# Performance work log

Hardware: AMD Instinct MI355X
Metric: run time of the kernel (lower is better)

## Reference

```python
import jax, jax.numpy as jnp
import numpy as np

B, T, V = 4096, 32, 256          # batch, decode steps, vocab
E, CE, H, L, NH = 768, 64, 256, 2, 4  # eword_dim, char_emb_dim, hidden, gru layers, heads
HD = H // NH                      # head dim
BOS, PAD = 1, 0


def _gru_cell(x, h, w_ih, w_hh, b_ih, b_hh):
    # PyTorch GRUCell math: gates ordered (r, z, n)
    gi = x @ w_ih.T + b_ih
    gh = h @ w_hh.T + b_hh
    ir, iz, inn = jnp.split(gi, 3, axis=-1)
    hr, hz, hn = jnp.split(gh, 3, axis=-1)
    r = jax.nn.sigmoid(ir + hr)
    z = jax.nn.sigmoid(iz + hz)
    n = jnp.tanh(inn + r * hn)
    return (1.0 - z) * n + z * h


def setup_inputs() -> dict:
    key = jax.random.key(0)
    ks = jax.random.split(key, 24)
    s = 0.02
    p = lambda k, shp: (jax.random.normal(k, shp, jnp.float32) * s)
    return {
        "eword": jax.random.normal(ks[0], (B, E), jnp.float32),
        "target_ids": jax.random.randint(ks[1], (B, T), 0, V),
        # params
        "char_emb": p(ks[2], (V, CE)).at[PAD].set(0.0),
        "eword_proj_w": p(ks[3], (H, E)), "eword_proj_b": p(ks[4], (H,)),
        "gru_w_ih0": p(ks[5], (3 * H, CE + E)), "gru_w_hh0": p(ks[6], (3 * H, H)),
        "gru_b_ih0": p(ks[7], (3 * H,)), "gru_b_hh0": p(ks[8], (3 * H,)),
        "gru_w_ih1": p(ks[9], (3 * H, H)), "gru_w_hh1": p(ks[10], (3 * H, H)),
        "gru_b_ih1": p(ks[11], (3 * H,)), "gru_b_hh1": p(ks[12], (3 * H,)),
        "attn_in_w": p(ks[13], (3 * H, H)), "attn_in_b": p(ks[14], (3 * H,)),
        "attn_out_w": p(ks[15], (H, H)), "attn_out_b": p(ks[16], (H,)),
        "key_w": p(ks[17], (H, E)), "key_b": p(ks[18], (H,)),
        "val_w": p(ks[19], (H, E)), "val_b": p(ks[20], (H,)),
        "proj_w": p(ks[21], (V, H)), "proj_b": p(ks[22], (V,)),
    }


def reference(eword, target_ids, char_emb, eword_proj_w, eword_proj_b,
              gru_w_ih0, gru_w_hh0, gru_b_ih0, gru_b_hh0,
              gru_w_ih1, gru_w_hh1, gru_b_ih1, gru_b_hh1,
              attn_in_w, attn_in_b, attn_out_w, attn_out_b,
              key_w, key_b, val_w, val_b, proj_w, proj_b):
    batch = eword.shape[0]
    # init hidden: tanh(Linear(eword)) broadcast across layers
    h0 = jnp.tanh(eword @ eword_proj_w.T + eword_proj_b)
    # pre-projected key/value (seq len 1), then MHA in-proj for k,v (static)
    wq, wk, wv = jnp.split(attn_in_w, 3, axis=0)
    bq, bk, bv = jnp.split(attn_in_b, 3)
    ek = (eword @ key_w.T + key_b) @ wk.T + bk        # (B, H)
    ev = (eword @ val_w.T + val_b) @ wv.T + bv        # (B, H)
    kh = ek.reshape(batch, NH, HD)                     # (B, NH, HD)
    vh = ev.reshape(batch, NH, HD)
    scale = 1.0 / np.sqrt(HD).astype(np.float32)

    # teacher forcing: input at step t is BOS for t=0, else target_ids[:, t-1]
    in_ids = jnp.concatenate(
        [jnp.full((batch, 1), BOS, target_ids.dtype), target_ids[:, :-1]], axis=1)

    def step(carry, ids):
        h_l0, h_l1 = carry
        ce = char_emb[ids] * (ids != PAD)[:, None].astype(char_emb.dtype)
        x = jnp.concatenate([ce, eword], axis=-1)     # (B, CE+E)
        h_l0 = _gru_cell(x, h_l0, gru_w_ih0, gru_w_hh0, gru_b_ih0, gru_b_hh0)
        h_l1 = _gru_cell(h_l0, h_l1, gru_w_ih1, gru_w_hh1, gru_b_ih1, gru_b_hh1)
        # single-query cross-attention over a length-1 key/value
        q = (h_l1 @ wq.T + bq).reshape(batch, NH, HD)
        score = jnp.sum(q * kh, axis=-1, keepdims=True) * scale  # (B, NH, 1)
        w = jax.nn.softmax(score, axis=-1)            # ones (len-1 softmax)
        attn = (w * vh).reshape(batch, H)
        attn_out = attn @ attn_out_w.T + attn_out_b
        out = h_l1 + attn_out
        logits = out @ proj_w.T + proj_b              # (B, V)
        return (h_l0, h_l1), logits

    _, logits_t = jax.lax.scan(step, (h0, h0), in_ids.T)  # (T, B, V)
    return jnp.transpose(logits_t, (1, 0, 2))              # (B, T, V)
```

## Files before the change

kernel.cpp:

```cpp
#include <hip/hip_runtime.h>


typedef __bf16 bf16;
typedef __attribute__((ext_vector_type(8))) __bf16 bf16x8;
typedef __attribute__((ext_vector_type(4))) __bf16 bf16x4;
typedef __attribute__((ext_vector_type(4))) float fx4;

#define MFMA16(a, b, c) __builtin_amdgcn_mfma_f32_16x16x32_bf16(a, b, c, 0, 0, 0)

__device__ __forceinline__ float sigm(float x) { return 1.0f / (1.0f + expf(-x)); }

__device__ __forceinline__ bf16x8 cvt8(const float* __restrict__ p) {
    float4 u = ((const float4*)p)[0];
    float4 v = ((const float4*)p)[1];
    bf16x8 r;
    r[0] = (bf16)u.x; r[1] = (bf16)u.y; r[2] = (bf16)u.z; r[3] = (bf16)u.w;
    r[4] = (bf16)v.x; r[5] = (bf16)v.y; r[6] = (bf16)v.z; r[7] = (bf16)v.w;
    return r;
}

__device__ __forceinline__ bf16x8 addcvt8(bf16x8 h, const float* __restrict__ p) {
    float4 u = ((const float4*)p)[0];
    float4 v = ((const float4*)p)[1];
    bf16x8 r;
    r[0] = (bf16)((float)h[0] + u.x); r[1] = (bf16)((float)h[1] + u.y);
    r[2] = (bf16)((float)h[2] + u.z); r[3] = (bf16)((float)h[3] + u.w);
    r[4] = (bf16)((float)h[4] + v.x); r[5] = (bf16)((float)h[5] + v.y);
    r[6] = (bf16)((float)h[6] + v.z); r[7] = (bf16)((float)h[7] + v.w);
    return r;
}

__global__ void f2b(const float* __restrict__ s, bf16* __restrict__ d, int n) {
    int i = (blockIdx.x * 256 + threadIdx.x) * 4;
    if (i >= n) return;
    float4 v = *(const float4*)(s + i);
    bf16x4 o;
    o[0] = (bf16)v.x; o[1] = (bf16)v.y; o[2] = (bf16)v.z; o[3] = (bf16)v.w;
    *(bf16x4*)(d + i) = o;
}

__global__ __launch_bounds__(256, 4) void gemm_bt(
    const float* __restrict__ A, int lda,
    const float* __restrict__ W, int ldw,
    const float* __restrict__ bias,
    float* __restrict__ out, int ldo, int act_tanh, int K)
{
    const int tid  = threadIdx.x;
    const int wid  = tid >> 6;
    const int lane = tid & 63;
    const int quad = lane >> 4;
    const int l16  = lane & 15;
    const int m0   = blockIdx.x * 32;
    const int n0   = blockIdx.y * 256 + wid * 64;

    fx4 acc[4][2];
#pragma unroll
    for (int j = 0; j < 4; ++j) {
        acc[j][0] = fx4{0.f, 0.f, 0.f, 0.f};
        acc[j][1] = fx4{0.f, 0.f, 0.f, 0.f};
    }

    const float* a0p = A + (size_t)(m0 + l16) * lda + quad * 8;
    const float* a1p = A + (size_t)(m0 + 16 + l16) * lda + quad * 8;

    for (int k0 = 0; k0 < K; k0 += 32) {
        bf16x8 a0 = cvt8(a0p + k0);
        bf16x8 a1 = cvt8(a1p + k0);
#pragma unroll
        for (int j = 0; j < 4; ++j) {
            bf16x8 b = cvt8(W + (size_t)(n0 + j * 16 + l16) * ldw + k0 + quad * 8);
            acc[j][0] = MFMA16(a0, b, acc[j][0]);
            acc[j][1] = MFMA16(a1, b, acc[j][1]);
        }
    }

#pragma unroll
    for (int j = 0; j < 4; ++j) {
        int n = n0 + j * 16 + l16;
        float bv = bias ? bias[n] : 0.0f;
#pragma unroll
        for (int rt = 0; rt < 2; ++rt)
#pragma unroll
            for (int r = 0; r < 4; ++r) {
                int m = m0 + rt * 16 + quad * 4 + r;
                float v = acc[j][rt][r] + bv;
                if (act_tanh) v = tanhf(v);
                out[(size_t)m * ldo + n] = v;
            }
    }
}

__global__ __launch_bounds__(1024) void decoder_loop(
    const int*   __restrict__ tgt,
    const float* __restrict__ h0i,
    const float* __restrict__ gword,
    const float* __restrict__ cproj,
    const bf16*  __restrict__ w_hh0, const float* __restrict__ b_hh0,
    const bf16*  __restrict__ w_ih1, const float* __restrict__ b_ih1,
    const bf16*  __restrict__ w_hh1, const float* __restrict__ b_hh1,
    bf16* __restrict__ h1all)
{
    __shared__ __align__(16) bf16 hb0[2][16][264];
    __shared__ __align__(16) bf16 hb1[2][16][264];

    const int tid  = threadIdx.x;
    const int wid  = tid >> 6;
    const int lane = tid & 63;
    const int quad = lane >> 4;
    const int l16  = lane & 15;
    const int row0 = blockIdx.x * 16;
    const int col  = wid * 16 + l16;

    float h0m[4], h1m[4], gwv[3][4], cpv[3][4];
    float bh0[3], bi1[3], bh1[3];
#pragma unroll
    for (int g = 0; g < 3; ++g) {
        bh0[g] = b_hh0[g * 256 + col];
        bi1[g] = b_ih1[g * 256 + col];
        bh1[g] = b_hh1[g * 256 + col];
    }
#pragma unroll
    for (int r = 0; r < 4; ++r) {
        int lrow = quad * 4 + r;
        float v = h0i[(size_t)(row0 + lrow) * 256 + col];
        h0m[r] = v; h1m[r] = v;
        bf16 bv = (bf16)v;
        hb0[0][lrow][col] = bv; hb1[0][lrow][col] = bv;
#pragma unroll
        for (int g = 0; g < 3; ++g)
            gwv[g][r] = gword[(size_t)(row0 + lrow) * 768 + g * 256 + col];
    }
#pragma unroll
    for (int g = 0; g < 3; ++g) {
        float v = cproj[768 + g * 256 + col];
#pragma unroll
        for (int r = 0; r < 4; ++r) cpv[g][r] = v;
    }

    int woff[3];
#pragma unroll
    for (int g = 0; g < 3; ++g)
        woff[g] = ((g * 256 + col) * 256 + quad * 8) * 2;

    __syncthreads();

    for (int t = 0; t < 32; ++t) {
        const int p = t & 1, q = p ^ 1;

        fx4 g0[3], g1[3];
#pragma unroll
        for (int g = 0; g < 3; ++g) {
            g0[g] = fx4{0.f, 0.f, 0.f, 0.f};
            g1[g] = fx4{0.f, 0.f, 0.f, 0.f};
        }
#pragma unroll
        for (int k0 = 0; k0 < 256; k0 += 32) {
            bf16x8 a0 = *(const bf16x8*)&hb0[p][l16][k0 + quad * 8];
            bf16x8 c0 = *(const bf16x8*)&hb1[p][l16][k0 + quad * 8];
#pragma unroll
            for (int g = 0; g < 3; ++g) {
                bf16x8 b0 = *(const bf16x8*)((const char*)w_hh0 + woff[g] + k0 * 2);
                g0[g] = MFMA16(a0, b0, g0[g]);
                bf16x8 b1 = *(const bf16x8*)((const char*)w_hh1 + woff[g] + k0 * 2);
                g1[g] = MFMA16(c0, b1, g1[g]);
            }
        }
#pragma unroll
        for (int r = 0; r < 4; ++r) {
            float rr = sigm(cpv[0][r] + gwv[0][r] + g0[0][r] + bh0[0]);
            float zz = sigm(cpv[1][r] + gwv[1][r] + g0[1][r] + bh0[1]);
            float nn = tanhf(cpv[2][r] + gwv[2][r] + rr * (g0[2][r] + bh0[2]));
            h0m[r] = (1.0f - zz) * nn + zz * h0m[r];
            hb0[q][quad * 4 + r][col] = (bf16)h0m[r];
        }
        __syncthreads();

        int nid[4];
#pragma unroll
        for (int r = 0; r < 4; ++r)
            nid[r] = tgt[(row0 + quad * 4 + r) * 32 + t];
#pragma unroll
        for (int g = 0; g < 3; ++g)
#pragma unroll
            for (int r = 0; r < 4; ++r)
                cpv[g][r] = cproj[(size_t)nid[r] * 768 + g * 256 + col];

        fx4 gi[3];
#pragma unroll
        for (int g = 0; g < 3; ++g) gi[g] = fx4{0.f, 0.f, 0.f, 0.f};
#pragma unroll
        for (int k0 = 0; k0 < 256; k0 += 32) {
            bf16x8 a = *(const bf16x8*)&hb0[q][l16][k0 + quad * 8];
#pragma unroll
            for (int g = 0; g < 3; ++g) {
                bf16x8 b = *(const bf16x8*)((const char*)w_ih1 + woff[g] + k0 * 2);
                gi[g] = MFMA16(a, b, gi[g]);
            }
        }
#pragma unroll
        for (int r = 0; r < 4; ++r) {
            float rr = sigm(gi[0][r] + bi1[0] + g1[0][r] + bh1[0]);
            float zz = sigm(gi[1][r] + bi1[1] + g1[1][r] + bh1[1]);
            float nn = tanhf(gi[2][r] + bi1[2] + rr * (g1[2][r] + bh1[2]));
            h1m[r] = (1.0f - zz) * nn + zz * h1m[r];
            bf16 hv = (bf16)h1m[r];
            hb1[q][quad * 4 + r][col] = hv;
            h1all[((size_t)(row0 + quad * 4 + r) * 32 + t) * 256 + col] = hv;
        }
        __syncthreads();
    }
}

__global__ __launch_bounds__(256, 4) void logits_final(
    const bf16*  __restrict__ h1,
    const float* __restrict__ a2,
    const bf16*  __restrict__ pw,
    const float* __restrict__ pb,
    float* __restrict__ out)
{
    const int tid  = threadIdx.x;
    const int wid  = tid >> 6;
    const int lane = tid & 63;
    const int quad = lane >> 4;
    const int l16  = lane & 15;
    const int m0   = blockIdx.x * 32;
    const int n0   = wid * 64;
    const int b    = m0 >> 5;

    fx4 acc[4][2];
#pragma unroll
    for (int j = 0; j < 4; ++j) {
        acc[j][0] = fx4{0.f, 0.f, 0.f, 0.f};
        acc[j][1] = fx4{0.f, 0.f, 0.f, 0.f};
    }

    for (int k0 = 0; k0 < 256; k0 += 32) {
        bf16x8 h0 = *(const bf16x8*)(h1 + (size_t)(m0 + l16) * 256 + k0 + quad * 8);
        bf16x8 h1v = *(const bf16x8*)(h1 + (size_t)(m0 + 16 + l16) * 256 + k0 + quad * 8);
        const float* ap = a2 + (size_t)b * 256 + k0 + quad * 8;
        bf16x8 a0 = addcvt8(h0, ap);
        bf16x8 a1 = addcvt8(h1v, ap);
#pragma unroll
        for (int j = 0; j < 4; ++j) {
            bf16x8 bb = *(const bf16x8*)(pw + (size_t)(n0 + j * 16 + l16) * 256 + k0 + quad * 8);
            acc[j][0] = MFMA16(a0, bb, acc[j][0]);
            acc[j][1] = MFMA16(a1, bb, acc[j][1]);
        }
    }

#pragma unroll
    for (int j = 0; j < 4; ++j) {
        int n = n0 + j * 16 + l16;
        float bv = pb[n];
#pragma unroll
        for (int rt = 0; rt < 2; ++rt)
#pragma unroll
            for (int r = 0; r < 4; ++r) {
                int m = m0 + rt * 16 + quad * 4 + r;
                out[(size_t)m * 256 + n] = acc[j][rt][r] + bv;
            }
    }
}

extern "C" void kernel_launch(void* const* d_in, const int* in_sizes, int n_in,
                              void* d_out, int out_size, void* d_ws, size_t ws_size,
                              hipStream_t stream)
{
    const float* eword      = (const float*)d_in[0];
    const int*   tgt        = (const int*)  d_in[1];
    const float* char_emb   = (const float*)d_in[2];
    const float* ew_w       = (const float*)d_in[3];
    const float* ew_b       = (const float*)d_in[4];
    const float* w_ih0      = (const float*)d_in[5];
    const float* w_hh0      = (const float*)d_in[6];
    const float* b_ih0      = (const float*)d_in[7];
    const float* b_hh0      = (const float*)d_in[8];
    const float* w_ih1      = (const float*)d_in[9];
    const float* w_hh1      = (const float*)d_in[10];
    const float* b_ih1      = (const float*)d_in[11];
    const float* b_hh1      = (const float*)d_in[12];
    const float* attn_in_w  = (const float*)d_in[13];
    const float* attn_in_b  = (const float*)d_in[14];
    const float* attn_out_w = (const float*)d_in[15];
    const float* attn_out_b = (const float*)d_in[16];
    const float* val_w      = (const float*)d_in[19];
    const float* val_b      = (const float*)d_in[20];
    const float* proj_w     = (const float*)d_in[21];
    const float* proj_b     = (const float*)d_in[22];

    char* ws = (char*)d_ws;
    float* h0i   = (float*)ws;  ws += (size_t)4096 * 256 * 4;
    float* gwrd  = (float*)ws;  ws += (size_t)4096 * 768 * 4;
    float* cproj = (float*)ws;  ws += (size_t)256  * 768 * 4;
    float* a2    = (float*)ws;  ws += (size_t)4096 * 256 * 4;
    float* buf1  = (float*)ws;  ws += (size_t)4096 * 256 * 4;
    float* buf2  = (float*)ws;  ws += (size_t)4096 * 256 * 4;
    bf16*  wbhh0 = (bf16*)ws;   ws += (size_t)768 * 256 * 2;
    bf16*  wbih1 = (bf16*)ws;   ws += (size_t)768 * 256 * 2;
    bf16*  wbhh1 = (bf16*)ws;   ws += (size_t)768 * 256 * 2;
    bf16*  wbprj = (bf16*)ws;   ws += (size_t)256 * 256 * 2;
    bf16*  h1all = (bf16*)ws;   ws += (size_t)4096 * 32 * 256 * 2;

    dim3 blk(256);
    f2b<<<dim3(192), blk, 0, stream>>>(w_hh0, wbhh0, 768 * 256);
    f2b<<<dim3(192), blk, 0, stream>>>(w_ih1, wbih1, 768 * 256);
    f2b<<<dim3(192), blk, 0, stream>>>(w_hh1, wbhh1, 768 * 256);
    f2b<<<dim3(64),  blk, 0, stream>>>(proj_w, wbprj, 256 * 256);

    gemm_bt<<<dim3(128, 1), blk, 0, stream>>>(eword, 768, ew_w, 768, ew_b, h0i, 256, 1, 768);
    gemm_bt<<<dim3(128, 3), blk, 0, stream>>>(eword, 768, w_ih0 + 64, 832, b_ih0, gwrd, 768, 0, 768);
    gemm_bt<<<dim3(8, 3),   blk, 0, stream>>>(char_emb, 64, w_ih0, 832, nullptr, cproj, 768, 0, 64);
    gemm_bt<<<dim3(128, 1), blk, 0, stream>>>(eword, 768, val_w, 768, val_b, buf1, 256, 0, 768);
    gemm_bt<<<dim3(128, 1), blk, 0, stream>>>(buf1, 256, attn_in_w + 512 * 256, 256, attn_in_b + 512, buf2, 256, 0, 256);
    gemm_bt<<<dim3(128, 1), blk, 0, stream>>>(buf2, 256, attn_out_w, 256, attn_out_b, a2, 256, 0, 256);

    decoder_loop<<<dim3(256), dim3(1024), 0, stream>>>(
        tgt, h0i, gwrd, cproj,
        wbhh0, b_hh0, wbih1, b_ih1, wbhh1, b_hh1, h1all);

    logits_final<<<dim3(4096), blk, 0, stream>>>(h1all, a2, wbprj, proj_b, (float*)d_out);
}
```

Baseline: 2.170 ms.

## Partition decoder by hidden columns with LDS-resident weight slices and cross-block flag sync

The decoder loop changes from one block per 16 batch rows, each streaming all GRU weights from global memory every step, to blocks that each own a 16-column slice of all three recurrent weight matrices held in swizzled LDS. Each block covers 256 rows. Hidden states now go through double-buffered global memory, and a cooperative launch with per-row-group atomic counters acts as a barrier between the layer-0 and layer-1 phases. The aim is to remove the repeated global and L2 weight traffic per step, at the cost of global hidden-state round trips and spin-wait synchronisation across blocks.

```diff
diff --git a/kernel.cpp b/kernel.cpp
--- a/kernel.cpp
+++ b/kernel.cpp
@@ -37,6 +37,11 @@
     bf16x4 o;
     o[0] = (bf16)v.x; o[1] = (bf16)v.y; o[2] = (bf16)v.z; o[3] = (bf16)v.w;
     *(bf16x4*)(d + i) = o;
+}
+
+__global__ void zero_u32(unsigned* __restrict__ p, int n) {
+    int i = blockIdx.x * 256 + threadIdx.x;
+    if (i < n) p[i] = 0u;
 }
 
 __global__ __launch_bounds__(256, 4) void gemm_bt(
@@ -90,7 +95,7 @@
     }
 }
 
-__global__ __launch_bounds__(1024) void decoder_loop(
+__global__ __launch_bounds__(1024, 4) void decoder_loop(
     const int*   __restrict__ tgt,
     const float* __restrict__ h0i,
     const float* __restrict__ gword,
@@ -98,55 +103,86 @@
     const bf16*  __restrict__ w_hh0, const float* __restrict__ b_hh0,
     const bf16*  __restrict__ w_ih1, const float* __restrict__ b_ih1,
     const bf16*  __restrict__ w_hh1, const float* __restrict__ b_hh1,
+    bf16* __restrict__ h0g,
+    bf16* __restrict__ h1g,
+    unsigned* __restrict__ c0f,
+    unsigned* __restrict__ c1f,
     bf16* __restrict__ h1all)
 {
-    __shared__ __align__(16) bf16 hb0[2][16][264];
-    __shared__ __align__(16) bf16 hb1[2][16][264];
+    __shared__ __align__(16) bf16 wlds[3 * 48 * 256];
 
     const int tid  = threadIdx.x;
-    const int wid  = tid >> 6;
+    const int wv   = tid >> 6;
     const int lane = tid & 63;
     const int quad = lane >> 4;
     const int l16  = lane & 15;
-    const int row0 = blockIdx.x * 16;
-    const int col  = wid * 16 + l16;
+    const int bid  = blockIdx.x;
+    const int rg   = (bid & 7) * 2 + ((bid >> 3) & 1);
+    const int cg   = bid >> 4;
+    const int R0   = rg * 256 + wv * 16;
+    const int colg = cg * 16 + l16;
+    const int rowc = rg * 256 + wv * 16 + quad * 4;
+    const int xw   = (l16 & 7) << 3;
+    const size_t HSZ = (size_t)4096 * 256;
+
+    const bf16* Ws[3] = { w_hh0, w_ih1, w_hh1 };
+#pragma unroll
+    for (int m = 0; m < 3; ++m)
+        for (int v = tid; v < 1536; v += 1024) {
+            int lr = v >> 5, k8 = v & 31;
+            int g = lr >> 4, c = lr & 15;
+            bf16x8 w = *(const bf16x8*)(Ws[m] + (size_t)(g * 256 + cg * 16 + c) * 256 + k8 * 8);
+            *(bf16x8*)&wlds[(m * 48 + lr) * 256 + ((k8 * 8) ^ ((lr & 7) << 3))] = w;
+        }
 
     float h0m[4], h1m[4], gwv[3][4], cpv[3][4];
     float bh0[3], bi1[3], bh1[3];
 #pragma unroll
     for (int g = 0; g < 3; ++g) {
-        bh0[g] = b_hh0[g * 256 + col];
-        bi1[g] = b_ih1[g * 256 + col];
-        bh1[g] = b_hh1[g * 256 + col];
+        bh0[g] = b_hh0[g * 256 + colg];
+        bi1[g] = b_ih1[g * 256 + colg];
+        bh1[g] = b_hh1[g * 256 + colg];
     }
 #pragma unroll
     for (int r = 0; r < 4; ++r) {
-        int lrow = quad * 4 + r;
-        float v = h0i[(size_t)(row0 + lrow) * 256 + col];
+        int row = rowc + r;
+        float v = h0i[(size_t)row * 256 + colg];
         h0m[r] = v; h1m[r] = v;
         bf16 bv = (bf16)v;
-        hb0[0][lrow][col] = bv; hb1[0][lrow][col] = bv;
+        h0g[(size_t)row * 256 + colg] = bv;
+        h1g[(size_t)row * 256 + colg] = bv;
 #pragma unroll
         for (int g = 0; g < 3; ++g)
-            gwv[g][r] = gword[(size_t)(row0 + lrow) * 768 + g * 256 + col];
+            gwv[g][r] = gword[(size_t)row * 768 + g * 256 + colg];
     }
 #pragma unroll
     for (int g = 0; g < 3; ++g) {
-        float v = cproj[768 + g * 256 + col];
+        float v = cproj[768 + g * 256 + colg];
 #pragma unroll
         for (int r = 0; r < 4; ++r) cpv[g][r] = v;
     }
 
-    int woff[3];
-#pragma unroll
-    for (int g = 0; g < 3; ++g)
-        woff[g] = ((g * 256 + col) * 256 + quad * 8) * 2;
-
     __syncthreads();
+    if (tid == 0) {
+        __threadfence();
+        __hip_atomic_fetch_add(&c0f[rg * 32], 1u, __ATOMIC_RELEASE, __HIP_MEMORY_SCOPE_AGENT);
+        __hip_atomic_fetch_add(&c1f[rg * 32], 1u, __ATOMIC_RELEASE, __HIP_MEMORY_SCOPE_AGENT);
+    }
 
     for (int t = 0; t < 32; ++t) {
         const int p = t & 1, q = p ^ 1;
 
+        if (tid == 0) {
+            unsigned tv = 16u * (unsigned)(t + 1);
+            while (__hip_atomic_load(&c0f[rg * 32], __ATOMIC_ACQUIRE, __HIP_MEMORY_SCOPE_AGENT) < tv)
+                __builtin_amdgcn_s_sleep(2);
+            while (__hip_atomic_load(&c1f[rg * 32], __ATOMIC_ACQUIRE, __HIP_MEMORY_SCOPE_AGENT) < tv)
+                __builtin_amdgcn_s_sleep(2);
+        }
+        __syncthreads();
+
+        const bf16* h0p = h0g + p * HSZ + (size_t)(R0 + l16) * 256 + quad * 8;
+        const bf16* h1p = h1g + p * HSZ + (size_t)(R0 + l16) * 256 + quad * 8;
         fx4 g0[3], g1[3];
 #pragma unroll
         for (int g = 0; g < 3; ++g) {
@@ -154,15 +190,16 @@
             g1[g] = fx4{0.f, 0.f, 0.f, 0.f};
         }
 #pragma unroll
-        for (int k0 = 0; k0 < 256; k0 += 32) {
-            bf16x8 a0 = *(const bf16x8*)&hb0[p][l16][k0 + quad * 8];
-            bf16x8 c0 = *(const bf16x8*)&hb1[p][l16][k0 + quad * 8];
+        for (int kk = 0; kk < 8; ++kk) {
+            bf16x8 a = *(const bf16x8*)(h0p + kk * 32);
+            bf16x8 c = *(const bf16x8*)(h1p + kk * 32);
+            int kb = (kk * 32 + quad * 8) ^ xw;
 #pragma unroll
             for (int g = 0; g < 3; ++g) {
-                bf16x8 b0 = *(const bf16x8*)((const char*)w_hh0 + woff[g] + k0 * 2);
-                g0[g] = MFMA16(a0, b0, g0[g]);
-                bf16x8 b1 = *(const bf16x8*)((const char*)w_hh1 + woff[g] + k0 * 2);
-                g1[g] = MFMA16(c0, b1, g1[g]);
+                bf16x8 b0 = *(const bf16x8*)&wlds[(0 * 48 + g * 16 + l16) * 256 + kb];
+                g0[g] = MFMA16(a, b0, g0[g]);
+                bf16x8 b2 = *(const bf16x8*)&wlds[(2 * 48 + g * 16 + l16) * 256 + kb];
+                g1[g] = MFMA16(c, b2, g1[g]);
             }
         }
 #pragma unroll
@@ -171,29 +208,43 @@
             float zz = sigm(cpv[1][r] + gwv[1][r] + g0[1][r] + bh0[1]);
             float nn = tanhf(cpv[2][r] + gwv[2][r] + rr * (g0[2][r] + bh0[2]));
             h0m[r] = (1.0f - zz) * nn + zz * h0m[r];
-            hb0[q][quad * 4 + r][col] = (bf16)h0m[r];
+            h0g[q * HSZ + (size_t)(rowc + r) * 256 + colg] = (bf16)h0m[r];
         }
         __syncthreads();
-
+        if (tid == 0) {
+            __threadfence();
+            __hip_atomic_fetch_add(&c0f[rg * 32], 1u, __ATOMIC_RELEASE, __HIP_MEMORY_SCOPE_AGENT);
+        }
+
+        float cpn[3][4];
         int nid[4];
 #pragma unroll
         for (int r = 0; r < 4; ++r)
-            nid[r] = tgt[(row0 + quad * 4 + r) * 32 + t];
+            nid[r] = tgt[(rowc + r) * 32 + t];
 #pragma unroll
         for (int g = 0; g < 3; ++g)
 #pragma unroll
             for (int r = 0; r < 4; ++r)
-                cpv[g][r] = cproj[(size_t)nid[r] * 768 + g * 256 + col];
-
+                cpn[g][r] = cproj[(size_t)nid[r] * 768 + g * 256 + colg];
+
+        if (tid == 0) {
+            unsigned tv = 16u * (unsigned)(t + 2);
+            while (__hip_atomic_load(&c0f[rg * 32], __ATOMIC_ACQUIRE, __HIP_MEMORY_SCOPE_AGENT) < tv)
+                __builtin_amdgcn_s_sleep(2);
+        }
+        __syncthreads();
+
+        const bf16* h0q = h0g + q * HSZ + (size_t)(R0 + l16) * 256 + quad * 8;
         fx4 gi[3];
 #pragma unroll
         for (int g = 0; g < 3; ++g) gi[g] = fx4{0.f, 0.f, 0.f, 0.f};
 #pragma unroll
-        for (int k0 = 0; k0 < 256; k0 += 32) {
-            bf16x8 a = *(const bf16x8*)&hb0[q][l16][k0 + quad * 8];
+        for (int kk = 0; kk < 8; ++kk) {
+            bf16x8 a = *(const bf16x8*)(h0q + kk * 32);
+            int kb = (kk * 32 + quad * 8) ^ xw;
 #pragma unroll
             for (int g = 0; g < 3; ++g) {
-                bf16x8 b = *(const bf16x8*)((const char*)w_ih1 + woff[g] + k0 * 2);
+                bf16x8 b = *(const bf16x8*)&wlds[(1 * 48 + g * 16 + l16) * 256 + kb];
                 gi[g] = MFMA16(a, b, gi[g]);
             }
         }
@@ -204,10 +255,19 @@
             float nn = tanhf(gi[2][r] + bi1[2] + rr * (g1[2][r] + bh1[2]));
             h1m[r] = (1.0f - zz) * nn + zz * h1m[r];
             bf16 hv = (bf16)h1m[r];
-            hb1[q][quad * 4 + r][col] = hv;
-            h1all[((size_t)(row0 + quad * 4 + r) * 32 + t) * 256 + col] = hv;
-        }
+            h1g[q * HSZ + (size_t)(rowc + r) * 256 + colg] = hv;
+            h1all[((size_t)(rowc + r) * 32 + t) * 256 + colg] = hv;
+        }
+#pragma unroll
+        for (int g = 0; g < 3; ++g)
+#pragma unroll
+            for (int r = 0; r < 4; ++r) cpv[g][r] = cpn[g][r];
+
         __syncthreads();
+        if (tid == 0) {
+            __threadfence();
+            __hip_atomic_fetch_add(&c1f[rg * 32], 1u, __ATOMIC_RELEASE, __HIP_MEMORY_SCOPE_AGENT);
+        }
     }
 }
 
@@ -293,19 +353,25 @@
     float* gwrd  = (float*)ws;  ws += (size_t)4096 * 768 * 4;
     float* cproj = (float*)ws;  ws += (size_t)256  * 768 * 4;
     float* a2    = (float*)ws;  ws += (size_t)4096 * 256 * 4;
-    float* buf1  = (float*)ws;  ws += (size_t)4096 * 256 * 4;
-    float* buf2  = (float*)ws;  ws += (size_t)4096 * 256 * 4;
+    char*  hreg  = ws;          ws += (size_t)8 * 1024 * 1024;
+    float* buf1  = (float*)hreg;
+    float* buf2  = (float*)(hreg + (size_t)4*1024*1024);
+    bf16*  h0g   = (bf16*)hreg;
+    bf16*  h1g   = (bf16*)(hreg + (size_t)4*1024*1024);
     bf16*  wbhh0 = (bf16*)ws;   ws += (size_t)768 * 256 * 2;
     bf16*  wbih1 = (bf16*)ws;   ws += (size_t)768 * 256 * 2;
     bf16*  wbhh1 = (bf16*)ws;   ws += (size_t)768 * 256 * 2;
     bf16*  wbprj = (bf16*)ws;   ws += (size_t)256 * 256 * 2;
     bf16*  h1all = (bf16*)ws;   ws += (size_t)4096 * 32 * 256 * 2;
+    unsigned* c0f = (unsigned*)ws; ws += 16 * 32 * 4;
+    unsigned* c1f = (unsigned*)ws; ws += 16 * 32 * 4;
 
     dim3 blk(256);
     f2b<<<dim3(192), blk, 0, stream>>>(w_hh0, wbhh0, 768 * 256);
     f2b<<<dim3(192), blk, 0, stream>>>(w_ih1, wbih1, 768 * 256);
     f2b<<<dim3(192), blk, 0, stream>>>(w_hh1, wbhh1, 768 * 256);
     f2b<<<dim3(64),  blk, 0, stream>>>(proj_w, wbprj, 256 * 256);
+    zero_u32<<<dim3(4), blk, 0, stream>>>(c0f, 2 * 16 * 32);
 
     gemm_bt<<<dim3(128, 1), blk, 0, stream>>>(eword, 768, ew_w, 768, ew_b, h0i, 256, 1, 768);
     gemm_bt<<<dim3(128, 3), blk, 0, stream>>>(eword, 768, w_ih0 + 64, 832, b_ih0, gwrd, 768, 0, 768);
@@ -314,9 +380,16 @@
     gemm_bt<<<dim3(128, 1), blk, 0, stream>>>(buf1, 256, attn_in_w + 512 * 256, 256, attn_in_b + 512, buf2, 256, 0, 256);
     gemm_bt<<<dim3(128, 1), blk, 0, stream>>>(buf2, 256, attn_out_w, 256, attn_out_b, a2, 256, 0, 256);
 
-    decoder_loop<<<dim3(256), dim3(1024), 0, stream>>>(
-        tgt, h0i, gwrd, cproj,
-        wbhh0, b_hh0, wbih1, b_ih1, wbhh1, b_hh1, h1all);
+    {
+        void* kargs[] = {
+            (void*)&tgt, (void*)&h0i, (void*)&gwrd, (void*)&cproj,
+            (void*)&wbhh0, (void*)&b_hh0, (void*)&wbih1, (void*)&b_ih1,
+            (void*)&wbhh1, (void*)&b_hh1,
+            (void*)&h0g, (void*)&h1g, (void*)&c0f, (void*)&c1f, (void*)&h1all
+        };
+        hipLaunchCooperativeKernel((const void*)decoder_loop, dim3(256), dim3(1024),
+                                   kargs, 0, stream);
+    }
 
     logits_final<<<dim3(4096), blk, 0, stream>>>(h1all, a2, wbprj, proj_b, (float*)d_out);
 }
```

Result: slower. 2.228 ms (+2.7%).

## Software-pipeline weight and hidden-state loads in GRU decoder loop

Applied to the files above, without the earlier changes.

Restructures the recurrent decoder's MFMA inner loops to double-buffer weight fragments from global memory and hidden-state fragments from LDS two steps ahead, so load latency overlaps with matrix math. It also pre-adds the char-projection and eword gate contributions into one register array, moves the target-id load to the top of the step, uses nontemporal stores for the h1 history, and adds a min-blocks hint to launch bounds. The extra prefetch registers raise register pressure, and the launch-bounds hint can force spills in a 1024-thread block.

```diff
diff --git a/kernel.cpp b/kernel.cpp
--- a/kernel.cpp
+++ b/kernel.cpp
@@ -90,7 +90,7 @@
     }
 }
 
-__global__ __launch_bounds__(1024) void decoder_loop(
+__global__ __launch_bounds__(1024, 4) void decoder_loop(
     const int*   __restrict__ tgt,
     const float* __restrict__ h0i,
     const float* __restrict__ gword,
@@ -110,8 +110,9 @@
     const int l16  = lane & 15;
     const int row0 = blockIdx.x * 16;
     const int col  = wid * 16 + l16;
-
-    float h0m[4], h1m[4], gwv[3][4], cpv[3][4];
+    const int rw   = quad * 4;
+
+    float h0m[4], h1m[4], cg[3][4];
     float bh0[3], bi1[3], bh1[3];
 #pragma unroll
     for (int g = 0; g < 3; ++g) {
@@ -121,22 +122,20 @@
     }
 #pragma unroll
     for (int r = 0; r < 4; ++r) {
-        int lrow = quad * 4 + r;
-        float v = h0i[(size_t)(row0 + lrow) * 256 + col];
+        int row = row0 + rw + r;
+        float v = h0i[(size_t)row * 256 + col];
         h0m[r] = v; h1m[r] = v;
         bf16 bv = (bf16)v;
-        hb0[0][lrow][col] = bv; hb1[0][lrow][col] = bv;
+        hb0[0][rw + r][col] = bv; hb1[0][rw + r][col] = bv;
 #pragma unroll
         for (int g = 0; g < 3; ++g)
-            gwv[g][r] = gword[(size_t)(row0 + lrow) * 768 + g * 256 + col];
-    }
-#pragma unroll
-    for (int g = 0; g < 3; ++g) {
-        float v = cproj[768 + g * 256 + col];
-#pragma unroll
-        for (int r = 0; r < 4; ++r) cpv[g][r] = v;
-    }
-
+            cg[g][r] = cproj[(size_t)768 + g * 256 + col]
+                     + gword[(size_t)row * 768 + g * 256 + col];
+    }
+
+    const char* Wp0 = (const char*)w_hh0;
+    const char* Wp1 = (const char*)w_ih1;
+    const char* Wp2 = (const char*)w_hh1;
     int woff[3];
 #pragma unroll
     for (int g = 0; g < 3; ++g)
@@ -146,6 +145,11 @@
 
     for (int t = 0; t < 32; ++t) {
         const int p = t & 1, q = p ^ 1;
+
+        int nid[4];
+#pragma unroll
+        for (int r = 0; r < 4; ++r)
+            nid[r] = tgt[(row0 + rw + r) * 32 + t];
 
         fx4 g0[3], g1[3];
 #pragma unroll
@@ -153,48 +157,75 @@
             g0[g] = fx4{0.f, 0.f, 0.f, 0.f};
             g1[g] = fx4{0.f, 0.f, 0.f, 0.f};
         }
-#pragma unroll
-        for (int k0 = 0; k0 < 256; k0 += 32) {
-            bf16x8 a0 = *(const bf16x8*)&hb0[p][l16][k0 + quad * 8];
-            bf16x8 c0 = *(const bf16x8*)&hb1[p][l16][k0 + quad * 8];
+        bf16x8 av[2], cv[2], wb0[2], wb2[2];
+        av[0] = *(const bf16x8*)&hb0[p][l16][quad * 8];
+        cv[0] = *(const bf16x8*)&hb1[p][l16][quad * 8];
+        av[1] = *(const bf16x8*)&hb0[p][l16][32 + quad * 8];
+        cv[1] = *(const bf16x8*)&hb1[p][l16][32 + quad * 8];
+        wb0[0] = *(const bf16x8*)(Wp0 + woff[0]);
+        wb2[0] = *(const bf16x8*)(Wp2 + woff[0]);
+        wb0[1] = *(const bf16x8*)(Wp0 + woff[1]);
+        wb2[1] = *(const bf16x8*)(Wp2 + woff[1]);
+#pragma unroll
+        for (int kk = 0; kk < 8; ++kk) {
+            bf16x8 au = av[kk & 1], cu = cv[kk & 1];
+            if (kk < 6) {
+                av[kk & 1] = *(const bf16x8*)&hb0[p][l16][(kk + 2) * 32 + quad * 8];
+                cv[kk & 1] = *(const bf16x8*)&hb1[p][l16][(kk + 2) * 32 + quad * 8];
+            }
 #pragma unroll
             for (int g = 0; g < 3; ++g) {
-                bf16x8 b0 = *(const bf16x8*)((const char*)w_hh0 + woff[g] + k0 * 2);
-                g0[g] = MFMA16(a0, b0, g0[g]);
-                bf16x8 b1 = *(const bf16x8*)((const char*)w_hh1 + woff[g] + k0 * 2);
-                g1[g] = MFMA16(c0, b1, g1[g]);
+                const int s = kk * 3 + g;
+                bf16x8 b0 = wb0[s & 1], b2 = wb2[s & 1];
+                if (s + 2 < 24) {
+                    const int g2 = (s + 2) % 3, k2 = (s + 2) / 3;
+                    wb0[s & 1] = *(const bf16x8*)(Wp0 + woff[g2] + k2 * 64);
+                    wb2[s & 1] = *(const bf16x8*)(Wp2 + woff[g2] + k2 * 64);
+                }
+                g0[g] = MFMA16(au, b0, g0[g]);
+                g1[g] = MFMA16(cu, b2, g1[g]);
             }
         }
 #pragma unroll
         for (int r = 0; r < 4; ++r) {
-            float rr = sigm(cpv[0][r] + gwv[0][r] + g0[0][r] + bh0[0]);
-            float zz = sigm(cpv[1][r] + gwv[1][r] + g0[1][r] + bh0[1]);
-            float nn = tanhf(cpv[2][r] + gwv[2][r] + rr * (g0[2][r] + bh0[2]));
+            float rr = sigm(cg[0][r] + g0[0][r] + bh0[0]);
+            float zz = sigm(cg[1][r] + g0[1][r] + bh0[1]);
+            float nn = tanhf(cg[2][r] + rr * (g0[2][r] + bh0[2]));
             h0m[r] = (1.0f - zz) * nn + zz * h0m[r];
-            hb0[q][quad * 4 + r][col] = (bf16)h0m[r];
+            hb0[q][rw + r][col] = (bf16)h0m[r];
         }
         __syncthreads();
 
-        int nid[4];
-#pragma unroll
-        for (int r = 0; r < 4; ++r)
-            nid[r] = tgt[(row0 + quad * 4 + r) * 32 + t];
+        float cgn[3][4];
 #pragma unroll
         for (int g = 0; g < 3; ++g)
 #pragma unroll
             for (int r = 0; r < 4; ++r)
-                cpv[g][r] = cproj[(size_t)nid[r] * 768 + g * 256 + col];
+                cgn[g][r] = cproj[(size_t)nid[r] * 768 + g * 256 + col]
+                          + gword[(size_t)(row0 + rw + r) * 768 + g * 256 + col];
 
         fx4 gi[3];
 #pragma unroll
         for (int g = 0; g < 3; ++g) gi[g] = fx4{0.f, 0.f, 0.f, 0.f};
-#pragma unroll
-        for (int k0 = 0; k0 < 256; k0 += 32) {
-            bf16x8 a = *(const bf16x8*)&hb0[q][l16][k0 + quad * 8];
+        bf16x8 bv2[2], wb1[2];
+        bv2[0] = *(const bf16x8*)&hb0[q][l16][quad * 8];
+        bv2[1] = *(const bf16x8*)&hb0[q][l16][32 + quad * 8];
+        wb1[0] = *(const bf16x8*)(Wp1 + woff[0]);
+        wb1[1] = *(const bf16x8*)(Wp1 + woff[1]);
+#pragma unroll
+        for (int kk = 0; kk < 8; ++kk) {
+            bf16x8 au = bv2[kk & 1];
+            if (kk < 6)
+                bv2[kk & 1] = *(const bf16x8*)&hb0[q][l16][(kk + 2) * 32 + quad * 8];
 #pragma unroll
             for (int g = 0; g < 3; ++g) {
-                bf16x8 b = *(const bf16x8*)((const char*)w_ih1 + woff[g] + k0 * 2);
-                gi[g] = MFMA16(a, b, gi[g]);
+                const int s = kk * 3 + g;
+                bf16x8 b = wb1[s & 1];
+                if (s + 2 < 24) {
+                    const int g2 = (s + 2) % 3, k2 = (s + 2) / 3;
+                    wb1[s & 1] = *(const bf16x8*)(Wp1 + woff[g2] + k2 * 64);
+                }
+                gi[g] = MFMA16(au, b, gi[g]);
             }
         }
 #pragma unroll
@@ -204,9 +235,15 @@
             float nn = tanhf(gi[2][r] + bi1[2] + rr * (g1[2][r] + bh1[2]));
             h1m[r] = (1.0f - zz) * nn + zz * h1m[r];
             bf16 hv = (bf16)h1m[r];
-            hb1[q][quad * 4 + r][col] = hv;
-            h1all[((size_t)(row0 + quad * 4 + r) * 32 + t) * 256 + col] = hv;
-        }
+            hb1[q][rw + r][col] = hv;
+            __builtin_nontemporal_store(
+                hv, &h1all[((size_t)(row0 + rw + r) * 32 + t) * 256 + col]);
+        }
+#pragma unroll
+        for (int g = 0; g < 3; ++g)
+#pragma unroll
+            for (int r = 0; r < 4; ++r) cg[g][r] = cgn[g][r];
+
         __syncthreads();
     }
 }
```

After: 2.263 ms. 1.04x slower.
